# Performance work log

Measured on AMD Instinct MI355X. Metric: run time of the kernel, lower is better.

## Reference

```python
import jax, jax.numpy as jnp
import numpy as np

N_EMBED = 1024
N_HEADS = 16
HEAD_DIM = N_EMBED // N_HEADS


def setup_inputs() -> dict:
    key = jax.random.key(0)
    ks = jax.random.split(key, 5)
    x = jax.random.normal(ks[0], (4, 2048, N_EMBED), dtype=jnp.float32)
    # Linear params stored as [in, out] (y = x @ W + b), math-equivalent to torch Linear
    scale_attn = 1.0 / np.sqrt(N_EMBED)
    W_attn = jax.random.normal(ks[1], (N_EMBED, 3 * N_EMBED), dtype=jnp.float32) * scale_attn
    b_attn = jax.random.normal(ks[2], (3 * N_EMBED,), dtype=jnp.float32) * 0.02
    W_proj = jax.random.normal(ks[3], (N_EMBED, N_EMBED), dtype=jnp.float32) * scale_attn
    b_proj = jax.random.normal(ks[4], (N_EMBED,), dtype=jnp.float32) * 0.02
    return {"x": x, "W_attn": W_attn, "b_attn": b_attn, "W_proj": W_proj, "b_proj": b_proj}


def reference(x, W_attn, b_attn, W_proj, b_proj):
    BS, SL, ED = x.shape
    qkv = x @ W_attn + b_attn                      # [B, S, 3E]
    q, k, v = jnp.split(qkv, 3, axis=2)
    # [B, H, S, D]
    def heads(t):
        return t.reshape(BS, SL, N_HEADS, HEAD_DIM).transpose(0, 2, 1, 3)
    q, k, v = heads(q), heads(k), heads(v)
    att = jnp.einsum('bhqd,bhkd->bhqk', q, k) * (HEAD_DIM ** -0.5)
    causal = jnp.tril(jnp.ones((SL, SL), dtype=bool))
    att = jnp.where(causal[None, None], att, -jnp.inf)
    att = jax.nn.softmax(att, axis=-1)
    y = jnp.einsum('bhqk,bhkd->bhqd', att, v)      # [B, H, S, D]
    y = y.transpose(0, 2, 1, 3).reshape(BS, SL, ED)
    return y @ W_proj + b_proj
```

## Files before the change

kernel.cpp:

```cpp
#include <hip/hip_runtime.h>


#define BATCH 4
#define SEQ   2048
#define EMB   1024
#define NH    16
#define HD    64

typedef __bf16 bf16;
typedef __bf16 bf16x8 __attribute__((ext_vector_type(8)));
typedef float  f32x4  __attribute__((ext_vector_type(4)));

__device__ __forceinline__ void ld_lds16(const void* g, void* l) {
  __builtin_amdgcn_global_load_lds(
      (const __attribute__((address_space(1))) void*)g,
      (__attribute__((address_space(3))) void*)l, 16, 0, 0);
}

__global__ void cvt_f32_bf16(const float* __restrict__ in, bf16* __restrict__ out, int n) {
  int i = (blockIdx.x * blockDim.x + threadIdx.x) * 4;
  if (i + 3 < n) {
    float4 v = *(const float4*)(in + i);
    bf16 o0 = (bf16)v.x, o1 = (bf16)v.y, o2 = (bf16)v.z, o3 = (bf16)v.w;
    out[i] = o0; out[i+1] = o1; out[i+2] = o2; out[i+3] = o3;
  }
}

__global__ void transpose_cvt2(const float* __restrict__ Wa, const float* __restrict__ Wp,
                               bf16* __restrict__ WaT, bf16* __restrict__ WpT) {
  __shared__ float tile[32][33];
  int bx = blockIdx.x;
  const float* W; bf16* WT; int N;
  if (bx < 96) { W = Wa; WT = WaT; N = 3072; }
  else         { W = Wp; WT = WpT; N = 1024; bx -= 96; }
  int n0 = bx * 32, k0 = blockIdx.y * 32;
  int tx = threadIdx.x & 31, ty = threadIdx.x >> 5;
#pragma unroll
  for (int r = 0; r < 4; r++) {
    int k = k0 + ty + r * 8;
    tile[ty + r * 8][tx] = W[(long)k * N + n0 + tx];
  }
  __syncthreads();
#pragma unroll
  for (int r = 0; r < 4; r++) {
    int n = n0 + ty + r * 8;
    WT[(long)n * EMB + k0 + tx] = (bf16)tile[tx][ty + r * 8];
  }
}

#define QSCALE 0.18033688f

__global__ __launch_bounds__(256, 2) void gemm8p(
    const bf16* __restrict__ A, const bf16* __restrict__ Bt,
    const float* __restrict__ bias,
    bf16* __restrict__ q, bf16* __restrict__ k, bf16* __restrict__ v)
{
  __shared__ __align__(16) bf16 lds[24576];
  int lin = blockIdx.x;
  int xcd = lin & 7, s = lin >> 3;
  int by = xcd * 8 + (s & 7);
  int bx = s >> 3;
  int m0 = by * 128, n0 = bx * 256;
  int t = threadIdx.x;
  int wid = t >> 6, lane = t & 63;
  int l15 = lane & 15, quad = lane >> 4;
  int wc = wid;

  const bf16* Ag = A + (long)m0 * EMB;
  const bf16* Bg = Bt + (long)n0 * EMB;

  f32x4 acc[8][4] = {};
  bf16x8 af[8], bfr[4];
  constexpr int NT = EMB / 32;
  int ph8 = ((quad + (l15 >> 1)) & 3) * 8;

#define LDSA(b) (lds + (b) * 4096)
#define LDSB(b) (lds + 8192 + (b) * 8192)

#define ISSUE64(gbase, rowoff, ldst, ktt)                                      \
  { int r_ = (rowoff) + (t >> 2);                                              \
    int g_ = ((t & 3) - ((t >> 3) & 3)) & 3;                                   \
    ld_lds16(&(gbase)[(long)r_ * EMB + (ktt) + g_ * 8],                        \
             (ldst) + ((rowoff) + wid * 16) * 32); }

#define RD_A(mi) { int r_ = (mi) * 16 + l15;                                   \
    af[mi] = *(const bf16x8*)&Ab[r_ * 32 + ph8]; }
#define RD_B(ni) { int r_ = wc * 64 + (ni) * 16 + l15;                         \
    bfr[ni] = *(const bf16x8*)&Bb[r_ * 32 + ph8]; }

#define FENCE asm volatile("" ::: "memory")
#define BAR   { FENCE; __builtin_amdgcn_s_barrier(); FENCE; }

#define MFMAC(nlo)                                                             \
  { __builtin_amdgcn_s_setprio(1);                                             \
    _Pragma("unroll") for (int mi_ = 0; mi_ < 8; ++mi_)                        \
      _Pragma("unroll") for (int nj_ = 0; nj_ < 2; ++nj_)                      \
        acc[mi_][(nlo) + nj_] = __builtin_amdgcn_mfma_f32_16x16x32_bf16(       \
            af[mi_], bfr[(nlo) + nj_], acc[mi_][(nlo) + nj_], 0, 0, 0);        \
    __builtin_amdgcn_s_setprio(0); }

  ISSUE64(Ag, 0,   LDSA(0), 0);
  ISSUE64(Ag, 64,  LDSA(0), 0);
  ISSUE64(Bg, 0,   LDSB(0), 0);
  ISSUE64(Bg, 64,  LDSB(0), 0);
  ISSUE64(Bg, 128, LDSB(0), 0);
  ISSUE64(Bg, 192, LDSB(0), 0);
  ISSUE64(Ag, 0,   LDSA(1), 32);
  asm volatile("s_waitcnt vmcnt(1)" ::: "memory");
  BAR;

#pragma unroll 2
  for (int tt = 0; tt < NT; ++tt) {
    const bf16* Ab = LDSA(tt & 1);
    const bf16* Bb = LDSB(tt & 1);
    bf16* An = LDSA((tt + 1) & 1);
    bf16* Bn = LDSB((tt + 1) & 1);
    bf16* Ac = LDSA(tt & 1);
    int kn  = (tt + 1 < NT ? tt + 1 : NT - 1) * 32;
    int kn2 = (tt + 2 < NT ? tt + 2 : NT - 1) * 32;

#pragma unroll
    for (int mi = 0; mi < 8; ++mi) RD_A(mi);
    RD_B(0); RD_B(1);
    ISSUE64(Ag, 64,  An, kn);
    ISSUE64(Bg, 0,   Bn, kn);
    ISSUE64(Bg, 64,  Bn, kn);
    ISSUE64(Bg, 128, Bn, kn);
    BAR; MFMAC(0); BAR;
    RD_B(2); RD_B(3);
    ISSUE64(Bg, 192, Bn, kn);
    ISSUE64(Ag, 0,   Ac, kn2);
    asm volatile("s_waitcnt vmcnt(1)" ::: "memory");
    BAR; MFMAC(2); BAR;
  }

  asm volatile("s_waitcnt vmcnt(0)" ::: "memory");
  __syncthreads();

  int which = bx >> 2;
  if (which < 2) {
    bf16* dst = (which == 0) ? q : k;
    float scale = (which == 0) ? QSCALE : 1.0f;
#pragma unroll
    for (int mi = 0; mi < 8; ++mi)
#pragma unroll
      for (int ni = 0; ni < 4; ++ni) {
        int gcol = n0 + wc * 64 + ni * 16 + l15;
        float bv = bias[gcol];
        int e = gcol & 1023, h = e >> 6, d = e & 63;
#pragma unroll
        for (int i = 0; i < 4; ++i) {
          int grow = m0 + mi * 16 + quad * 4 + i;
          int b = grow >> 11, ss = grow & 2047;
          dst[(((long)b * NH + h) * SEQ + ss) * HD + d] =
              (bf16)((acc[mi][ni][i] + bv) * scale);
        }
      }
  } else {
#pragma unroll
    for (int mi = 0; mi < 8; ++mi)
#pragma unroll
      for (int ni = 0; ni < 4; ++ni) {
        int gcol = n0 + wc * 64 + ni * 16 + l15;
        float bv = bias[gcol];
        int e = gcol & 1023, h = e >> 6, d = e & 63;
#pragma unroll
        for (int i = 0; i < 4; ++i) {
          int grow = m0 + mi * 16 + quad * 4 + i;
          int b = grow >> 11, ss = grow & 2047;
          v[(((long)b * NH + h) * HD + d) * SEQ + ss] =
              (bf16)(acc[mi][ni][i] + bv);
        }
      }
  }
#undef LDSA
#undef LDSB
#undef ISSUE64
#undef RD_A
#undef RD_B
#undef MFMAC
}

__global__ __launch_bounds__(256, 3) void gemm_proj(
    const bf16* __restrict__ A, const bf16* __restrict__ Bt,
    const float* __restrict__ bias, float* __restrict__ out)
{
  __shared__ __align__(16) bf16 Al[128 * 64];
  __shared__ __align__(16) bf16 Bl[64 * 64];
  int lin = blockIdx.x;
  int xcd = lin & 7, s = lin >> 3;
  int bx = s >> 3, by = xcd * 8 + (s & 7);
  int m0 = by * 128;
  int n0 = bx * 64;
  int t = threadIdx.x;
  int wave = t >> 6, lane = t & 63;
  int l15 = lane & 15, quad = lane >> 4;
  int wm = (wave & 1) * 64, wn = (wave >> 1) * 32;

  f32x4 acc[4][2] = {};

  for (int kt = 0; kt < EMB; kt += 64) {
    __syncthreads();
#pragma unroll
    for (int it = 0; it < 4; ++it) {
      int c = it * 256 + t;
      int row = c >> 3, u = c & 7;
      ld_lds16(&A[(long)(m0 + row) * EMB + kt + ((u ^ (row & 7)) * 8)],
               &Al[(it * 256 + wave * 64) * 8]);
    }
    {
      int c = t;
      int row = c >> 3, u = c & 7;
      ld_lds16(&Bt[(long)(n0 + row) * EMB + kt + ((u ^ (row & 7)) * 8)],
               &Bl[(wave * 64) * 8]);
      c = 256 + t;
      row = c >> 3; u = c & 7;
      ld_lds16(&Bt[(long)(n0 + row) * EMB + kt + ((u ^ (row & 7)) * 8)],
               &Bl[(256 + wave * 64) * 8]);
    }
    __syncthreads();
#pragma unroll
    for (int ks = 0; ks < 2; ++ks) {
      bf16x8 af[4], bfr[2];
#pragma unroll
      for (int i = 0; i < 4; ++i) {
        int r = wm + i * 16 + l15;
        af[i] = *(const bf16x8*)(&Al[r * 64 + (((ks * 4 + quad) ^ (r & 7)) * 8)]);
      }
#pragma unroll
      for (int i = 0; i < 2; ++i) {
        int r = wn + i * 16 + l15;
        bfr[i] = *(const bf16x8*)(&Bl[r * 64 + (((ks * 4 + quad) ^ (r & 7)) * 8)]);
      }
#pragma unroll
      for (int mi = 0; mi < 4; ++mi)
#pragma unroll
        for (int ni = 0; ni < 2; ++ni)
          acc[mi][ni] = __builtin_amdgcn_mfma_f32_16x16x32_bf16(af[mi], bfr[ni], acc[mi][ni], 0, 0, 0);
    }
  }

#pragma unroll
  for (int mi = 0; mi < 4; ++mi)
#pragma unroll
    for (int ni = 0; ni < 2; ++ni) {
      int gcol = n0 + wn + ni * 16 + l15;
      float bv = bias[gcol];
#pragma unroll
      for (int i = 0; i < 4; ++i) {
        int grow = m0 + wm + mi * 16 + quad * 4 + i;
        out[(long)grow * EMB + gcol] = acc[mi][ni][i] + bv;
      }
    }
}

#define LDP 72

__global__ __launch_bounds__(256, 4) void attn(
    const bf16* __restrict__ Q, const bf16* __restrict__ K,
    const bf16* __restrict__ Vt, bf16* __restrict__ Y)
{
  __shared__ __align__(16) bf16 Kl[64 * 64];
  __shared__ __align__(16) bf16 Vl[64 * 64];
  __shared__ __align__(16) bf16 Pl[4][32 * LDP];
  int L = blockIdx.x;
  int a = L >> 3;
  int hd = (L & 7) + 8 * (a & 7);
  int s2 = a >> 3;
  int v = (s2 < 8) ? (2 * s2) : (2 * (15 - s2) + 1);
  int q0 = (15 - v) * 128;
  int b = hd >> 4, h = hd & 15;
  const bf16* Qp  = Q  + (((long)b * NH + h) * SEQ) * HD;
  const bf16* Kp  = K  + (((long)b * NH + h) * SEQ) * HD;
  const bf16* Vtp = Vt + (((long)b * NH + h) * HD) * SEQ;
  int t = threadIdx.x, wave = t >> 6, lane = t & 63;
  int l15 = lane & 15, quad = lane >> 4;
  int wq0 = q0 + wave * 32;

  bf16x8 qf[2][2];
#pragma unroll
  for (int m = 0; m < 2; ++m) {
    const bf16* qrow = Qp + (long)(wq0 + m * 16 + l15) * HD + quad * 8;
    qf[m][0] = *(const bf16x8*)(qrow);
    qf[m][1] = *(const bf16x8*)(qrow + 32);
  }
  float lrow[2][4] = {};
  f32x4 oacc[2][4] = {};

  int ntiles = q0 / 64 + 2;
#pragma unroll 1
  for (int kt = 0; kt < ntiles; ++kt) {
    int k0 = kt * 64;
    __syncthreads();
#pragma unroll
    for (int it = 0; it < 2; ++it) {
      int cu = it * 256 + t;
      int row = cu >> 3, u = cu & 7;
      ld_lds16(&Kp[(long)(k0 + row) * HD + ((u ^ (row & 7)) * 8)],
               &Kl[(it * 256 + wave * 64) * 8]);
      ld_lds16(&Vtp[(long)row * SEQ + k0 + ((u ^ (row & 7)) * 8)],
               &Vl[(it * 256 + wave * 64) * 8]);
    }
    __syncthreads();
    if (k0 > wq0 + 31) continue;

    f32x4 sc[2][4] = {};
#pragma unroll
    for (int kk = 0; kk < 2; ++kk) {
#pragma unroll
      for (int ni = 0; ni < 4; ++ni) {
        int r = ni * 16 + l15, u = kk * 4 + quad;
        bf16x8 kfr = *(const bf16x8*)(&Kl[r * 64 + ((u ^ (r & 7)) * 8)]);
        sc[0][ni] = __builtin_amdgcn_mfma_f32_16x16x32_bf16(qf[0][kk], kfr, sc[0][ni], 0, 0, 0);
        sc[1][ni] = __builtin_amdgcn_mfma_f32_16x16x32_bf16(qf[1][kk], kfr, sc[1][ni], 0, 0, 0);
      }
    }

    bool full = (k0 + 63 <= wq0);
#pragma unroll
    for (int m = 0; m < 2; ++m) {
#pragma unroll
      for (int i = 0; i < 4; ++i) {
        int qr = wq0 + m * 16 + quad * 4 + i;
        float e[4];
#pragma unroll
        for (int ni = 0; ni < 4; ++ni) {
          float x = sc[m][ni][i];
          if (!full) x = (k0 + ni * 16 + l15 <= qr) ? x : -1e30f;
          e[ni] = __builtin_amdgcn_exp2f(x);
        }
        lrow[m][i] += (e[0] + e[1]) + (e[2] + e[3]);
        int prow = (m * 16 + quad * 4 + i) * LDP;
#pragma unroll
        for (int ni = 0; ni < 4; ++ni)
          Pl[wave][prow + ni * 16 + l15] = (bf16)e[ni];
      }
    }
    asm volatile("s_waitcnt lgkmcnt(0)" ::: "memory");
#pragma unroll
    for (int kk = 0; kk < 2; ++kk) {
      int kbase = kk * 32 + quad * 8;
      bf16x8 pf0 = *(const bf16x8*)(&Pl[wave][(l15) * LDP + kbase]);
      bf16x8 pf1 = *(const bf16x8*)(&Pl[wave][(16 + l15) * LDP + kbase]);
#pragma unroll
      for (int ni = 0; ni < 4; ++ni) {
        int dd = ni * 16 + l15, u = kk * 4 + quad;
        bf16x8 vf = *(const bf16x8*)(&Vl[dd * 64 + ((u ^ (dd & 7)) * 8)]);
        oacc[0][ni] = __builtin_amdgcn_mfma_f32_16x16x32_bf16(pf0, vf, oacc[0][ni], 0, 0, 0);
        oacc[1][ni] = __builtin_amdgcn_mfma_f32_16x16x32_bf16(pf1, vf, oacc[1][ni], 0, 0, 0);
      }
    }
  }
#pragma unroll
  for (int m = 0; m < 2; ++m) {
#pragma unroll
    for (int i = 0; i < 4; ++i) {
      float rs = lrow[m][i];
#pragma unroll
      for (int off = 8; off; off >>= 1) rs += __shfl_xor(rs, off, 16);
      float inv = 1.0f / rs;
      int qr = wq0 + m * 16 + quad * 4 + i;
      bf16* dst = Y + ((long)(b * SEQ + qr)) * EMB + h * HD;
#pragma unroll
      for (int ni = 0; ni < 4; ++ni)
        dst[ni * 16 + l15] = (bf16)(oacc[m][ni][i] * inv);
    }
  }
}

extern "C" void kernel_launch(void* const* d_in, const int* in_sizes, int n_in,
                              void* d_out, int out_size, void* d_ws, size_t ws_size,
                              hipStream_t stream) {
  const float* x      = (const float*)d_in[0];
  const float* W_attn = (const float*)d_in[1];
  const float* b_attn = (const float*)d_in[2];
  const float* W_proj = (const float*)d_in[3];
  const float* b_proj = (const float*)d_in[4];
  float* out = (float*)d_out;
  char* ws = (char*)d_ws;
  bf16* xb  = (bf16*)(ws);
  bf16* WaT = (bf16*)(ws + 16777216);
  bf16* WpT = (bf16*)(ws + 23068672);
  bf16* Qb  = (bf16*)(ws + 25165824);
  bf16* Kb  = (bf16*)(ws + 41943040);
  bf16* Vtb = (bf16*)(ws + 58720256);
  bf16* Yb  = (bf16*)(ws + 75497472);

  cvt_f32_bf16<<<8192, 256, 0, stream>>>(x, xb, BATCH * SEQ * EMB);
  transpose_cvt2<<<dim3(128, 32), 256, 0, stream>>>(W_attn, W_proj, WaT, WpT);
  gemm8p<<<768, 256, 0, stream>>>(xb, WaT, b_attn, Qb, Kb, Vtb);
  attn<<<1024, 256, 0, stream>>>(Qb, Kb, Vtb, Yb);
  gemm_proj<<<1024, 256, 0, stream>>>(Yb, WpT, b_proj, out);
}
```

Baseline: 251.5 us.

## Split attention blocks into paired 64-row query tiles processed in two passes

```diff
diff --git a/kernel.cpp b/kernel.cpp
--- a/kernel.cpp
+++ b/kernel.cpp
@@ -262,108 +262,101 @@
 {
   __shared__ __align__(16) bf16 Kl[64 * 64];
   __shared__ __align__(16) bf16 Vl[64 * 64];
-  __shared__ __align__(16) bf16 Pl[4][32 * LDP];
+  __shared__ __align__(16) bf16 Pl[4][16 * LDP];
   int L = blockIdx.x;
   int a = L >> 3;
   int hd = (L & 7) + 8 * (a & 7);
-  int s2 = a >> 3;
-  int v = (s2 < 8) ? (2 * s2) : (2 * (15 - s2) + 1);
-  int q0 = (15 - v) * 128;
+  int pr = a >> 3;
   int b = hd >> 4, h = hd & 15;
   const bf16* Qp  = Q  + (((long)b * NH + h) * SEQ) * HD;
   const bf16* Kp  = K  + (((long)b * NH + h) * SEQ) * HD;
   const bf16* Vtp = Vt + (((long)b * NH + h) * HD) * SEQ;
   int t = threadIdx.x, wave = t >> 6, lane = t & 63;
   int l15 = lane & 15, quad = lane >> 4;
-  int wq0 = q0 + wave * 32;
-
-  bf16x8 qf[2][2];
-#pragma unroll
-  for (int m = 0; m < 2; ++m) {
-    const bf16* qrow = Qp + (long)(wq0 + m * 16 + l15) * HD + quad * 8;
-    qf[m][0] = *(const bf16x8*)(qrow);
-    qf[m][1] = *(const bf16x8*)(qrow + 32);
-  }
-  float lrow[2][4] = {};
-  f32x4 oacc[2][4] = {};
-
-  int ntiles = q0 / 64 + 2;
+
 #pragma unroll 1
-  for (int kt = 0; kt < ntiles; ++kt) {
-    int k0 = kt * 64;
-    __syncthreads();
-#pragma unroll
-    for (int it = 0; it < 2; ++it) {
-      int cu = it * 256 + t;
-      int row = cu >> 3, u = cu & 7;
-      ld_lds16(&Kp[(long)(k0 + row) * HD + ((u ^ (row & 7)) * 8)],
-               &Kl[(it * 256 + wave * 64) * 8]);
-      ld_lds16(&Vtp[(long)row * SEQ + k0 + ((u ^ (row & 7)) * 8)],
-               &Vl[(it * 256 + wave * 64) * 8]);
-    }
-    __syncthreads();
-    if (k0 > wq0 + 31) continue;
-
-    f32x4 sc[2][4] = {};
-#pragma unroll
-    for (int kk = 0; kk < 2; ++kk) {
-#pragma unroll
-      for (int ni = 0; ni < 4; ++ni) {
-        int r = ni * 16 + l15, u = kk * 4 + quad;
-        bf16x8 kfr = *(const bf16x8*)(&Kl[r * 64 + ((u ^ (r & 7)) * 8)]);
-        sc[0][ni] = __builtin_amdgcn_mfma_f32_16x16x32_bf16(qf[0][kk], kfr, sc[0][ni], 0, 0, 0);
-        sc[1][ni] = __builtin_amdgcn_mfma_f32_16x16x32_bf16(qf[1][kk], kfr, sc[1][ni], 0, 0, 0);
-      }
-    }
-
-    bool full = (k0 + 63 <= wq0);
-#pragma unroll
-    for (int m = 0; m < 2; ++m) {
+  for (int pass = 0; pass < 2; ++pass) {
+    int sp = (pass == 0) ? (31 - pr) : pr;
+    int q0 = sp * 64;
+    int wq0 = q0 + wave * 16;
+
+    bf16x8 qf[2];
+    {
+      const bf16* qrow = Qp + (long)(wq0 + l15) * HD + quad * 8;
+      qf[0] = *(const bf16x8*)(qrow);
+      qf[1] = *(const bf16x8*)(qrow + 32);
+    }
+    float lrow[4] = {};
+    f32x4 oacc[4] = {};
+
+    int ntiles = sp + 1;
+#pragma unroll 1
+    for (int kt = 0; kt < ntiles; ++kt) {
+      int k0 = kt * 64;
+      __syncthreads();
+#pragma unroll
+      for (int it = 0; it < 2; ++it) {
+        int cu = it * 256 + t;
+        int row = cu >> 3, u = cu & 7;
+        ld_lds16(&Kp[(long)(k0 + row) * HD + ((u ^ (row & 7)) * 8)],
+                 &Kl[(it * 256 + wave * 64) * 8]);
+        ld_lds16(&Vtp[(long)row * SEQ + k0 + ((u ^ (row & 7)) * 8)],
+                 &Vl[(it * 256 + wave * 64) * 8]);
+      }
+      __syncthreads();
+
+      f32x4 sc[4] = {};
+#pragma unroll
+      for (int kk = 0; kk < 2; ++kk) {
+#pragma unroll
+        for (int ni = 0; ni < 4; ++ni) {
+          int r = ni * 16 + l15, u = kk * 4 + quad;
+          bf16x8 kfr = *(const bf16x8*)(&Kl[r * 64 + ((u ^ (r & 7)) * 8)]);
+          sc[ni] = __builtin_amdgcn_mfma_f32_16x16x32_bf16(qf[kk], kfr, sc[ni], 0, 0, 0);
+        }
+      }
+
+      bool full = (k0 + 63 <= wq0);
 #pragma unroll
       for (int i = 0; i < 4; ++i) {
-        int qr = wq0 + m * 16 + quad * 4 + i;
+        int qr = wq0 + quad * 4 + i;
         float e[4];
 #pragma unroll
         for (int ni = 0; ni < 4; ++ni) {
-          float x = sc[m][ni][i];
+          float x = sc[ni][i];
           if (!full) x = (k0 + ni * 16 + l15 <= qr) ? x : -1e30f;
           e[ni] = __builtin_amdgcn_exp2f(x);
         }
-        lrow[m][i] += (e[0] + e[1]) + (e[2] + e[3]);
-        int prow = (m * 16 + quad * 4 + i) * LDP;
+        lrow[i] += (e[0] + e[1]) + (e[2] + e[3]);
+        int prow = (quad * 4 + i) * LDP;
 #pragma unroll
         for (int ni = 0; ni < 4; ++ni)
           Pl[wave][prow + ni * 16 + l15] = (bf16)e[ni];
       }
-    }
-    asm volatile("s_waitcnt lgkmcnt(0)" ::: "memory");
-#pragma unroll
-    for (int kk = 0; kk < 2; ++kk) {
-      int kbase = kk * 32 + quad * 8;
-      bf16x8 pf0 = *(const bf16x8*)(&Pl[wave][(l15) * LDP + kbase]);
-      bf16x8 pf1 = *(const bf16x8*)(&Pl[wave][(16 + l15) * LDP + kbase]);
-#pragma unroll
-      for (int ni = 0; ni < 4; ++ni) {
-        int dd = ni * 16 + l15, u = kk * 4 + quad;
-        bf16x8 vf = *(const bf16x8*)(&Vl[dd * 64 + ((u ^ (dd & 7)) * 8)]);
-        oacc[0][ni] = __builtin_amdgcn_mfma_f32_16x16x32_bf16(pf0, vf, oacc[0][ni], 0, 0, 0);
-        oacc[1][ni] = __builtin_amdgcn_mfma_f32_16x16x32_bf16(pf1, vf, oacc[1][ni], 0, 0, 0);
-      }
-    }
-  }
-#pragma unroll
-  for (int m = 0; m < 2; ++m) {
+      asm volatile("s_waitcnt lgkmcnt(0)" ::: "memory");
+#pragma unroll
+      for (int kk = 0; kk < 2; ++kk) {
+        int kbase = kk * 32 + quad * 8;
+        bf16x8 pf = *(const bf16x8*)(&Pl[wave][(l15) * LDP + kbase]);
+#pragma unroll
+        for (int ni = 0; ni < 4; ++ni) {
+          int dd = ni * 16 + l15, u = kk * 4 + quad;
+          bf16x8 vf = *(const bf16x8*)(&Vl[dd * 64 + ((u ^ (dd & 7)) * 8)]);
+          oacc[ni] = __builtin_amdgcn_mfma_f32_16x16x32_bf16(pf, vf, oacc[ni], 0, 0, 0);
+        }
+      }
+    }
 #pragma unroll
     for (int i = 0; i < 4; ++i) {
-      float rs = lrow[m][i];
+      float rs = lrow[i];
 #pragma unroll
       for (int off = 8; off; off >>= 1) rs += __shfl_xor(rs, off, 16);
       float inv = 1.0f / rs;
-      int qr = wq0 + m * 16 + quad * 4 + i;
+      int qr = wq0 + quad * 4 + i;
       bf16* dst = Y + ((long)(b * SEQ + qr)) * EMB + h * HD;
 #pragma unroll
       for (int ni = 0; ni < 4; ++ni)
-        dst[ni * 16 + l15] = (bf16)(oacc[m][ni][i] * inv);
+        dst[ni * 16 + l15] = (bf16)(oacc[ni][i] * inv);
     }
   }
 }
```

Result: no change. 248.2 us (-1.3%).
